# Performance work log

Measured on AMD Instinct MI355X. Metric: run time of the kernel, lower is better.

The kernel has to match this reference:

```python
import jax, jax.numpy as jnp
import numpy as np

IN_FEATURES = 4096
OUT_FEATURES = 11008
BATCH = 256


def unpack_i4(q):
    # q: [K//2, N] packed bytes; row 2k = low nibble, row 2k+1 = high nibble
    low = q & 15
    high = (q >> 4) & 15
    # interleave -> [K, N]
    return jnp.stack([low, high], axis=1).reshape(q.shape[0] * 2, q.shape[1])


def setup_inputs() -> dict:
    key = jax.random.key(0)
    k1, k2, k3, k4 = jax.random.split(key, 4)
    x = jax.random.normal(k1, (BATCH, IN_FEATURES), dtype=jnp.float32)
    qweight = jax.random.randint(k2, (IN_FEATURES // 2, OUT_FEATURES), 0, 256, dtype=jnp.int32)
    scales = jax.random.uniform(k3, (OUT_FEATURES,), dtype=jnp.float32)
    zeroes = jax.random.normal(k4, (OUT_FEATURES,), dtype=jnp.float32)
    return {"x": x, "qweight": qweight, "scales": scales, "zeroes": zeroes}


def reference(x, qweight, scales, zeroes):
    # Dequantize: per-output-channel scale/zero over unpacked int4 weights
    w = scales[None, :] * unpack_i4(qweight).astype(jnp.float32) - zeroes[None, :]  # [K, N]
    return x @ w  # [B, N]
```

## Files before the change

kernel.cpp:

```cpp
#include <hip/hip_runtime.h>
#include <stdint.h>

#define K_DIM 4096
#define N_DIM 11008
#define M_DIM 256

typedef uint32_t u32;
using frag_ab = __attribute__((ext_vector_type(8))) short;
using frag_cd = __attribute__((ext_vector_type(4))) float;
using u32x4   = __attribute__((ext_vector_type(4))) uint32_t;

typedef __attribute__((address_space(3))) const char lds_cc;

#define DSR128(dst, addr, off)                                       \
    asm volatile("ds_read_b128 %0, %1 offset:" #off                  \
                 : "=&v"(dst) : "v"(addr))
#define LGKM(n) do { asm volatile("s_waitcnt lgkmcnt(" #n ")" ::: "memory"); \
                     __builtin_amdgcn_sched_barrier(0); } while (0)
#define VMW(n) asm volatile("s_waitcnt vmcnt(" #n ")" ::: "memory")

__device__ __forceinline__ u32 f2bf_rn(float f) {
    u32 u = __builtin_bit_cast(u32, f);
    return (u + 0x7FFFu + ((u >> 16) & 1u)) >> 16;
}
__device__ __forceinline__ float bf2f(u32 b) {
    return __builtin_bit_cast(float, b << 16);
}
__device__ __forceinline__ void gll16(const void* g, void* l) {
    __builtin_amdgcn_global_load_lds(
        (const __attribute__((address_space(1))) u32*)g,
        (__attribute__((address_space(3))) u32*)l, 16, 0, 0);
}

#define BFCVT(q) ((u32)((__mul24((int)(q), 0x4004) & 0x003C003C) | 0x42004200))

__global__ __launch_bounds__(256) void prep_kernel(const float* __restrict__ x,
                                                   ushort* __restrict__ xbf,
                                                   float* __restrict__ rowsum) {
    const int row = blockIdx.x;
    const int tid = threadIdx.x;
    const float* xr = x + (size_t)row * K_DIM;
    ushort* br = xbf + (size_t)row * K_DIM;
    float s = 0.0f;
#pragma unroll
    for (int p = 0; p < 4; ++p) {
        int i = p * 1024 + tid * 4;
        float4 v = *reinterpret_cast<const float4*>(xr + i);
        u32 b0 = f2bf_rn(v.x), b1 = f2bf_rn(v.y), b2 = f2bf_rn(v.z), b3 = f2bf_rn(v.w);
        uint2 o;
        o.x = b0 | (b1 << 16);
        o.y = b2 | (b3 << 16);
        *reinterpret_cast<uint2*>(br + i) = o;
        s += bf2f(b0) + bf2f(b1) + bf2f(b2) + bf2f(b3);
    }
#pragma unroll
    for (int off = 32; off > 0; off >>= 1) s += __shfl_down(s, off, 64);
    __shared__ float wsum[4];
    if ((tid & 63) == 0) wsum[tid >> 6] = s;
    __syncthreads();
    if (tid == 0) rowsum[row] = wsum[0] + wsum[1] + wsum[2] + wsum[3];
}

__global__ __launch_bounds__(256, 3) void gemm_kernel(const int* __restrict__ qw,
                                                      const float* __restrict__ scales,
                                                      const float* __restrict__ zeroes,
                                                      const ushort* __restrict__ xbf,
                                                      const float* __restrict__ rowsum,
                                                      float* __restrict__ out,
                                                      ushort* __restrict__ partial,
                                                      int split4) {
    __shared__ uint4 Alds[3][512];
    __shared__ u32   Blds[3][2048];

    const u32* qwu = (const u32*)qw;
    const int tid  = threadIdx.x;
    const int lane = tid & 63;
    const int wid  = tid >> 6;
    const int l4   = lane & 15;
    const int c    = lane >> 4;

    const int orig = blockIdx.x;
    int nb, mb, sp, NTt;
    if (split4) {
        int wg = (orig & 7) * 86 + (orig >> 3);
        nb = wg >> 3; sp = (wg >> 1) & 3; mb = wg & 1; NTt = 32;
    } else {
        nb = orig >> 1; mb = orig & 1; sp = 0; NTt = 128;
    }
    const int n0 = nb * 128;
    const int m0 = mb * 128;
    const int wm = wid >> 1;
    const int wn = wid & 1;

    const ushort* asrc[2];
#pragma unroll
    for (int j = 0; j < 2; ++j)
        asrc[j] = xbf + (size_t)(m0 + j * 64 + wid * 16 + (lane >> 2)) * K_DIM +
                  sp * 1024 + 8 * ((lane & 3) ^ ((lane >> 3) & 3));
    const u32* bsrc[2];
#pragma unroll
    for (int r = 0; r < 2; ++r)
        bsrc[r] = qwu + (size_t)(sp * 512 + r * 8 + wid * 2 + (lane >> 5)) * N_DIM +
                  n0 + ((lane >> 4) & 1) * 64 + 4 * (lane & 15);

    const u32 aoff = (u32)((wm * 64 + l4) * 64 + ((c ^ ((l4 >> 1) & 3)) << 4));
    const u32 boff = (u32)(c * 2048 + wn * 256 + l4 * 16);

    frag_cd acc[4][4];
#pragma unroll
    for (int i = 0; i < 4; ++i)
#pragma unroll
        for (int j = 0; j < 4; ++j)
            acc[i][j] = (frag_cd){0.f, 0.f, 0.f, 0.f};

    auto stage = [&](int t, int buf) {
#pragma unroll
        for (int j = 0; j < 2; ++j)
            gll16(asrc[j] + (size_t)t * 32, &Alds[buf][j * 256 + wid * 64]);
#pragma unroll
        for (int r = 0; r < 2; ++r)
            gll16(bsrc[r] + (size_t)t * 16 * N_DIM,
                  &Blds[buf][(r * 256 + wid * 64) * 4]);
    };

    auto compute = [&](int buf) {
        lds_cc* Ab = (lds_cc*)&Alds[buf][0];
        lds_cc* Bb = (lds_cc*)&Blds[buf][0];
        u32x4 bqp[4];
        DSR128(bqp[0], Bb + boff, 0);
        DSR128(bqp[1], Bb + boff, 512);
        DSR128(bqp[2], Bb + boff, 1024);
        DSR128(bqp[3], Bb + boff, 1536);
        frag_ab afr[4];
        DSR128(afr[0], Ab + aoff, 0);
        DSR128(afr[1], Ab + aoff, 1024);
        DSR128(afr[2], Ab + aoff, 2048);
        DSR128(afr[3], Ab + aoff, 3072);
        LGKM(4);
        union { frag_ab f; u32 u[4]; } bb[4];
#pragma unroll
        for (int j = 0; j < 4; ++j) {
            bb[j].u[0] = BFCVT(bqp[0][j]);
            bb[j].u[1] = BFCVT(bqp[1][j]);
            bb[j].u[2] = BFCVT(bqp[2][j]);
            bb[j].u[3] = BFCVT(bqp[3][j]);
        }
        LGKM(3);
#pragma unroll
        for (int j = 0; j < 4; ++j)
            acc[0][j] = __builtin_amdgcn_mfma_f32_16x16x32_bf16(
                afr[0], bb[j].f, acc[0][j], 0, 0, 0);
        LGKM(2);
#pragma unroll
        for (int j = 0; j < 4; ++j)
            acc[1][j] = __builtin_amdgcn_mfma_f32_16x16x32_bf16(
                afr[1], bb[j].f, acc[1][j], 0, 0, 0);
        LGKM(1);
#pragma unroll
        for (int j = 0; j < 4; ++j)
            acc[2][j] = __builtin_amdgcn_mfma_f32_16x16x32_bf16(
                afr[2], bb[j].f, acc[2][j], 0, 0, 0);
        LGKM(0);
#pragma unroll
        for (int j = 0; j < 4; ++j)
            acc[3][j] = __builtin_amdgcn_mfma_f32_16x16x32_bf16(
                afr[3], bb[j].f, acc[3][j], 0, 0, 0);
    };

    stage(0, 0);

    int cur = 0;
    for (int t = 0; t < NTt; ++t) {
        int pbuf = cur + 1; if (pbuf >= 3) pbuf -= 3;
        if (t + 1 < NTt) {
            stage(t + 1, pbuf);
            VMW(4);
        } else {
            VMW(0);
        }
        __builtin_amdgcn_s_barrier();
        __builtin_amdgcn_sched_barrier(0);
        compute(cur);
        ++cur; if (cur >= 3) cur -= 3;
    }

    const int ce = n0 + wn * 64 + 4 * l4;
    const float4 scv = *reinterpret_cast<const float4*>(&scales[ce]);
    const float4 zv  = *reinterpret_cast<const float4*>(&zeroes[ce]);
    const float sc[4] = {scv.x, scv.y, scv.z, scv.w};
    const float zp[4] = {zv.x + 32.0f * scv.x, zv.y + 32.0f * scv.y,
                         zv.z + 32.0f * scv.z, zv.w + 32.0f * scv.w};
    if (sp == 0) {
#pragma unroll
        for (int mf = 0; mf < 4; ++mf) {
            const float4 rs = *reinterpret_cast<const float4*>(
                &rowsum[m0 + wm * 64 + mf * 16 + c * 4]);
            const float rsa[4] = {rs.x, rs.y, rs.z, rs.w};
#pragma unroll
            for (int jr = 0; jr < 4; ++jr) {
                int m = m0 + wm * 64 + mf * 16 + c * 4 + jr;
                float4 o;
                o.x = sc[0] * acc[mf][0][jr] - zp[0] * rsa[jr];
                o.y = sc[1] * acc[mf][1][jr] - zp[1] * rsa[jr];
                o.z = sc[2] * acc[mf][2][jr] - zp[2] * rsa[jr];
                o.w = sc[3] * acc[mf][3][jr] - zp[3] * rsa[jr];
                *reinterpret_cast<float4*>(&out[(size_t)m * N_DIM + ce]) = o;
            }
        }
    } else {
        ushort* pb = partial + (size_t)(sp - 1) * M_DIM * N_DIM;
#pragma unroll
        for (int mf = 0; mf < 4; ++mf)
#pragma unroll
            for (int jr = 0; jr < 4; ++jr) {
                int m = m0 + wm * 64 + mf * 16 + c * 4 + jr;
                ushort4 o;
                o.x = (ushort)f2bf_rn(sc[0] * acc[mf][0][jr]);
                o.y = (ushort)f2bf_rn(sc[1] * acc[mf][1][jr]);
                o.z = (ushort)f2bf_rn(sc[2] * acc[mf][2][jr]);
                o.w = (ushort)f2bf_rn(sc[3] * acc[mf][3][jr]);
                *reinterpret_cast<ushort4*>(&pb[(size_t)m * N_DIM + ce]) = o;
            }
    }
}

__global__ __launch_bounds__(256) void reduce_kernel(float* __restrict__ out,
                                                     const ushort* __restrict__ partial) {
    const size_t NTOT = (size_t)M_DIM * N_DIM;
    size_t i = ((size_t)blockIdx.x * 256 + threadIdx.x) * 4;
    float4 o = *reinterpret_cast<float4*>(out + i);
    ushort4 a = *reinterpret_cast<const ushort4*>(partial + i);
    ushort4 b = *reinterpret_cast<const ushort4*>(partial + NTOT + i);
    ushort4 d = *reinterpret_cast<const ushort4*>(partial + 2 * NTOT + i);
    o.x += bf2f(a.x) + bf2f(b.x) + bf2f(d.x);
    o.y += bf2f(a.y) + bf2f(b.y) + bf2f(d.y);
    o.z += bf2f(a.z) + bf2f(b.z) + bf2f(d.z);
    o.w += bf2f(a.w) + bf2f(b.w) + bf2f(d.w);
    *reinterpret_cast<float4*>(out + i) = o;
}

extern "C" void kernel_launch(void* const* d_in, const int* in_sizes, int n_in,
                              void* d_out, int out_size, void* d_ws, size_t ws_size,
                              hipStream_t stream) {
    const float* x      = (const float*)d_in[0];
    const int*   qw     = (const int*)d_in[1];
    const float* scales = (const float*)d_in[2];
    const float* zeroes = (const float*)d_in[3];
    float* out = (float*)d_out;

    const size_t XBF_BYTES = (size_t)M_DIM * K_DIM * 2;
    const size_t RS_OFF    = XBF_BYTES;
    const size_t P_OFF     = XBF_BYTES + 4096;
    const size_t P_BYTES   = (size_t)3 * M_DIM * N_DIM * 2;

    ushort* xbf    = (ushort*)d_ws;
    float*  rowsum = (float*)((char*)d_ws + RS_OFF);
    ushort* part   = (ushort*)((char*)d_ws + P_OFF);

    const bool split4 = ws_size >= P_OFF + P_BYTES;

    prep_kernel<<<M_DIM, 256, 0, stream>>>(x, xbf, rowsum);
    if (split4) {
        gemm_kernel<<<688, 256, 0, stream>>>(qw, scales, zeroes, xbf, rowsum,
                                             out, part, 1);
        reduce_kernel<<<(M_DIM * N_DIM) / (256 * 4), 256, 0, stream>>>(out, part);
    } else {
        gemm_kernel<<<172, 256, 0, stream>>>(qw, scales, zeroes, xbf, rowsum,
                                             out, nullptr, 0);
    }
}
```

Measured before the change: 48.43 us.

## Fuse split-K reduction into GEMM via per-tile atomic completion counter

```diff
diff --git a/kernel.cpp b/kernel.cpp
--- a/kernel.cpp
+++ b/kernel.cpp
@@ -4,6 +4,7 @@
 #define K_DIM 4096
 #define N_DIM 11008
 #define M_DIM 256
+#define MN ((size_t)M_DIM * N_DIM)
 
 typedef uint32_t u32;
 using frag_ab = __attribute__((ext_vector_type(8))) short;
@@ -33,6 +34,10 @@
 }
 
 #define BFCVT(q) ((u32)((__mul24((int)(q), 0x4004) & 0x003C003C) | 0x42004200))
+
+__global__ __launch_bounds__(256) void init_kernel(u32* __restrict__ cnt) {
+    if (threadIdx.x < 172) cnt[threadIdx.x] = 0;
+}
 
 __global__ __launch_bounds__(256) void prep_kernel(const float* __restrict__ x,
                                                    ushort* __restrict__ xbf,
@@ -68,9 +73,11 @@
                                                       const float* __restrict__ rowsum,
                                                       float* __restrict__ out,
                                                       ushort* __restrict__ partial,
-                                                      int split4) {
+                                                      u32* __restrict__ cnt,
+                                                      int mode) {
     __shared__ uint4 Alds[3][512];
     __shared__ u32   Blds[3][2048];
+    __shared__ u32   s_done;
 
     const u32* qwu = (const u32*)qw;
     const int tid  = threadIdx.x;
@@ -81,7 +88,7 @@
 
     const int orig = blockIdx.x;
     int nb, mb, sp, NTt;
-    if (split4) {
+    if (mode != 0) {
         int wg = (orig & 7) * 86 + (orig >> 3);
         nb = wg >> 3; sp = (wg >> 1) & 3; mb = wg & 1; NTt = 32;
     } else {
@@ -190,7 +197,52 @@
     const float sc[4] = {scv.x, scv.y, scv.z, scv.w};
     const float zp[4] = {zv.x + 32.0f * scv.x, zv.y + 32.0f * scv.y,
                          zv.z + 32.0f * scv.z, zv.w + 32.0f * scv.w};
-    if (sp == 0) {
+
+    if (mode == 2) {
+        ushort* pb = partial + (size_t)sp * MN;
+#pragma unroll
+        for (int mf = 0; mf < 4; ++mf)
+#pragma unroll
+            for (int jr = 0; jr < 4; ++jr) {
+                int m = m0 + wm * 64 + mf * 16 + c * 4 + jr;
+                ushort4 o;
+                o.x = (ushort)f2bf_rn(sc[0] * acc[mf][0][jr]);
+                o.y = (ushort)f2bf_rn(sc[1] * acc[mf][1][jr]);
+                o.z = (ushort)f2bf_rn(sc[2] * acc[mf][2][jr]);
+                o.w = (ushort)f2bf_rn(sc[3] * acc[mf][3][jr]);
+                *reinterpret_cast<ushort4*>(&pb[(size_t)m * N_DIM + ce]) = o;
+            }
+        __syncthreads();
+        if (tid == 0) {
+            __threadfence();
+            s_done = atomicAdd(&cnt[nb * 2 + mb], 1u);
+        }
+        __syncthreads();
+        if (s_done == 3u) {
+            __threadfence();
+#pragma unroll
+            for (int mf = 0; mf < 4; ++mf) {
+                const float4 rs = *reinterpret_cast<const float4*>(
+                    &rowsum[m0 + wm * 64 + mf * 16 + c * 4]);
+                const float rsa[4] = {rs.x, rs.y, rs.z, rs.w};
+#pragma unroll
+                for (int jr = 0; jr < 4; ++jr) {
+                    int m = m0 + wm * 64 + mf * 16 + c * 4 + jr;
+                    size_t base = (size_t)m * N_DIM + ce;
+                    ushort4 p0 = *reinterpret_cast<const ushort4*>(&partial[0 * MN + base]);
+                    ushort4 p1 = *reinterpret_cast<const ushort4*>(&partial[1 * MN + base]);
+                    ushort4 p2 = *reinterpret_cast<const ushort4*>(&partial[2 * MN + base]);
+                    ushort4 p3 = *reinterpret_cast<const ushort4*>(&partial[3 * MN + base]);
+                    float4 o;
+                    o.x = bf2f(p0.x) + bf2f(p1.x) + bf2f(p2.x) + bf2f(p3.x) - zp[0] * rsa[jr];
+                    o.y = bf2f(p0.y) + bf2f(p1.y) + bf2f(p2.y) + bf2f(p3.y) - zp[1] * rsa[jr];
+                    o.z = bf2f(p0.z) + bf2f(p1.z) + bf2f(p2.z) + bf2f(p3.z) - zp[2] * rsa[jr];
+                    o.w = bf2f(p0.w) + bf2f(p1.w) + bf2f(p2.w) + bf2f(p3.w) - zp[3] * rsa[jr];
+                    *reinterpret_cast<float4*>(&out[base]) = o;
+                }
+            }
+        }
+    } else if (mode == 0 || sp == 0) {
 #pragma unroll
         for (int mf = 0; mf < 4; ++mf) {
             const float4 rs = *reinterpret_cast<const float4*>(
@@ -208,7 +260,7 @@
             }
         }
     } else {
-        ushort* pb = partial + (size_t)(sp - 1) * M_DIM * N_DIM;
+        ushort* pb = partial + (size_t)(sp - 1) * MN;
 #pragma unroll
         for (int mf = 0; mf < 4; ++mf)
 #pragma unroll
@@ -226,12 +278,11 @@
 
 __global__ __launch_bounds__(256) void reduce_kernel(float* __restrict__ out,
                                                      const ushort* __restrict__ partial) {
-    const size_t NTOT = (size_t)M_DIM * N_DIM;
     size_t i = ((size_t)blockIdx.x * 256 + threadIdx.x) * 4;
     float4 o = *reinterpret_cast<float4*>(out + i);
     ushort4 a = *reinterpret_cast<const ushort4*>(partial + i);
-    ushort4 b = *reinterpret_cast<const ushort4*>(partial + NTOT + i);
-    ushort4 d = *reinterpret_cast<const ushort4*>(partial + 2 * NTOT + i);
+    ushort4 b = *reinterpret_cast<const ushort4*>(partial + MN + i);
+    ushort4 d = *reinterpret_cast<const ushort4*>(partial + 2 * MN + i);
     o.x += bf2f(a.x) + bf2f(b.x) + bf2f(d.x);
     o.y += bf2f(a.y) + bf2f(b.y) + bf2f(d.y);
     o.z += bf2f(a.z) + bf2f(b.z) + bf2f(d.z);
@@ -251,21 +302,32 @@
     const size_t XBF_BYTES = (size_t)M_DIM * K_DIM * 2;
     const size_t RS_OFF    = XBF_BYTES;
     const size_t P_OFF     = XBF_BYTES + 4096;
-    const size_t P_BYTES   = (size_t)3 * M_DIM * N_DIM * 2;
+    const size_t P3_BYTES  = 3 * MN * 2;
+    const size_t P4_BYTES  = 4 * MN * 2;
+    const size_t CNT_OFF   = P_OFF + P4_BYTES;
+    const size_t CNT_BYTES = 256 * 4;
 
     ushort* xbf    = (ushort*)d_ws;
     float*  rowsum = (float*)((char*)d_ws + RS_OFF);
     ushort* part   = (ushort*)((char*)d_ws + P_OFF);
-
-    const bool split4 = ws_size >= P_OFF + P_BYTES;
+    u32*    cnt    = (u32*)((char*)d_ws + CNT_OFF);
+
+    int mode;
+    if (ws_size >= CNT_OFF + CNT_BYTES)      mode = 2;
+    else if (ws_size >= P_OFF + P3_BYTES)    mode = 1;
+    else                                     mode = 0;
 
     prep_kernel<<<M_DIM, 256, 0, stream>>>(x, xbf, rowsum);
-    if (split4) {
+    if (mode == 2) {
+        init_kernel<<<1, 256, 0, stream>>>(cnt);
         gemm_kernel<<<688, 256, 0, stream>>>(qw, scales, zeroes, xbf, rowsum,
-                                             out, part, 1);
-        reduce_kernel<<<(M_DIM * N_DIM) / (256 * 4), 256, 0, stream>>>(out, part);
+                                             out, part, cnt, 2);
+    } else if (mode == 1) {
+        gemm_kernel<<<688, 256, 0, stream>>>(qw, scales, zeroes, xbf, rowsum,
+                                             out, part, nullptr, 1);
+        reduce_kernel<<<(int)(MN / (256 * 4)), 256, 0, stream>>>(out, part);
     } else {
         gemm_kernel<<<172, 256, 0, stream>>>(qw, scales, zeroes, xbf, rowsum,
-                                             out, nullptr, 0);
-    }
-}
+                                             out, nullptr, nullptr, 0);
+    }
+}
```

Result: slower. 102.2 us (+111.1%).
